# Performance work log

Hardware: AMD Instinct MI355X
Metric: run time of the kernel (lower is better)

Reference implementation:

```python
import jax, jax.numpy as jnp
import numpy as np

D_MODEL = 1024
NHEAD = 16
NUM_KV = 4
D_K = D_MODEL // NHEAD          # 64
GROUP = NHEAD // NUM_KV          # 4 query heads per kv head
ROPE_BASE = 10000.0


def _rope(x, seq_len):
    """Apply rotary embedding. x: [B, h, S, d_k], positions 0..seq_len-1."""
    half = D_K // 2
    inv_freq = 1.0 / (ROPE_BASE ** (jnp.arange(0, D_K, 2, dtype=jnp.float32) / D_K))
    t = jnp.arange(seq_len, dtype=jnp.float32)
    freqs = jnp.outer(t, inv_freq)                      # [S, d_k/2]
    emb = jnp.concatenate([freqs, freqs], axis=-1)      # [S, d_k]
    cos, sin = jnp.cos(emb), jnp.sin(emb)               # broadcast over B, h
    x1, x2 = x[..., :half], x[..., half:]
    rot = jnp.concatenate([-x2, x1], axis=-1)
    return x * cos + rot * sin


def setup_inputs() -> dict:
    key = jax.random.key(0)
    ks = jax.random.split(key, 12)
    B, S = 2, 2048
    s_in = 1.0 / np.sqrt(D_MODEL)
    inp = {
        "query": jax.random.normal(ks[0], (B, S, D_MODEL), jnp.float32),
        "key":   jax.random.normal(ks[1], (B, S, D_MODEL), jnp.float32),
        "value": jax.random.normal(ks[2], (B, S, D_MODEL), jnp.float32),
        "Wq": jax.random.normal(ks[3], (D_MODEL, D_MODEL), jnp.float32) * s_in,
        "bq": jnp.zeros((D_MODEL,), jnp.float32),
        "Wk": jax.random.normal(ks[4], (NUM_KV * D_K, D_MODEL), jnp.float32) * s_in,
        "bk": jnp.zeros((NUM_KV * D_K,), jnp.float32),
        "Wv": jax.random.normal(ks[5], (NUM_KV * D_K, D_MODEL), jnp.float32) * s_in,
        "bv": jnp.zeros((NUM_KV * D_K,), jnp.float32),
        "Wo": jax.random.normal(ks[6], (D_MODEL, D_MODEL), jnp.float32) * s_in,
        "bo": jnp.zeros((D_MODEL,), jnp.float32),
    }
    return inp


def reference(query, key, value, Wq, bq, Wk, bk, Wv, bv, Wo, bo):
    B, S, _ = query.shape
    T = key.shape[1]
    # projections (torch Linear: x @ W^T + b)
    Q = (query @ Wq.T + bq).reshape(B, S, NHEAD, D_K).transpose(0, 2, 1, 3)   # [B,H,S,dk]
    K = (key   @ Wk.T + bk).reshape(B, T, NUM_KV, D_K).transpose(0, 2, 1, 3)  # [B,KV,T,dk]
    V = (value @ Wv.T + bv).reshape(B, T, NUM_KV, D_K).transpose(0, 2, 1, 3)
    # fused RoPE (start_pos = 0)
    Q = _rope(Q, S)
    K = _rope(K, T)
    # expand kv heads (repeat_interleave on head dim)
    Kr = jnp.repeat(K, GROUP, axis=1)   # [B,H,T,dk]
    Vr = jnp.repeat(V, GROUP, axis=1)
    scale = 1.0 / np.sqrt(D_K)
    scores = jnp.einsum("bhsd,bhtd->bhst", Q, Kr) * scale   # [B,H,S,T]
    attn = jax.nn.softmax(scores, axis=-1)                    # dropout = eval/no-op
    context = jnp.einsum("bhst,bhtd->bhsd", attn, Vr)        # [B,H,S,dk]
    context = context.transpose(0, 2, 1, 3).reshape(B, S, D_MODEL)
    return context @ Wo.T + bo
```

## Files before the change

### kernel.cpp

```cpp
#include <hip/hip_runtime.h>
#include <hip/hip_bf16.h>

typedef __hip_bfloat16 bf16;
typedef __attribute__((ext_vector_type(8))) short short8;
typedef __attribute__((ext_vector_type(4))) short short4v;
typedef __attribute__((ext_vector_type(4))) float f32x4;
typedef __attribute__((ext_vector_type(4))) float float4v;

static __device__ inline short f2bf(float f){
  __hip_bfloat16 h = __float2bfloat16(f);
  return *reinterpret_cast<short*>(&h);
}

static __device__ __forceinline__ unsigned cvt_pk_bf16(float lo, float hi){
  unsigned r;
  asm("v_cvt_pk_bf16_f32 %0, %1, %2" : "=v"(r) : "v"(lo), "v"(hi));
  return r;
}

static __device__ __forceinline__ float exp2_fast(float x){
  float r;
  asm("v_exp_f32 %0, %1" : "=v"(r) : "v"(x));
  return r;
}

static __device__ __forceinline__ float max3f(float a, float b, float c){
  float r;
  asm("v_max3_f32 %0, %1, %2, %3" : "=v"(r) : "v"(a), "v"(b), "v"(c));
  return r;
}

static __device__ inline short8 load8(const float* p){
  float4v a = *reinterpret_cast<const float4v*>(p);
  float4v b = *reinterpret_cast<const float4v*>(p + 4);
  short8 r;
  unsigned* u = reinterpret_cast<unsigned*>(&r);
  u[0] = cvt_pk_bf16(a[0], a[1]);
  u[1] = cvt_pk_bf16(a[2], a[3]);
  u[2] = cvt_pk_bf16(b[0], b[1]);
  u[3] = cvt_pk_bf16(b[2], b[3]);
  return r;
}
static __device__ inline short8 load8(const bf16* p){
  return *reinterpret_cast<const short8*>(p);
}

typedef __attribute__((address_space(1))) const unsigned int gas_u32;
typedef __attribute__((address_space(3))) unsigned int las_u32;
static __device__ __forceinline__ void gload16(const void* g, void* l){
  __builtin_amdgcn_global_load_lds((gas_u32*)g, (las_u32*)l, 16, 0, 0);
}

template<int N>
static __device__ __forceinline__ void vm_barrier(){
  if constexpr (N == 8) asm volatile("s_waitcnt vmcnt(8)" ::: "memory");
  else if constexpr (N == 4) asm volatile("s_waitcnt vmcnt(4)" ::: "memory");
  else asm volatile("s_waitcnt vmcnt(0)" ::: "memory");
  __builtin_amdgcn_s_barrier();
  __builtin_amdgcn_sched_barrier(0);
}

__global__ void rope_table_kernel(float* __restrict__ tab){
  const int idx = blockIdx.x * 256 + threadIdx.x;
  const int d = idx & 31, s = idx >> 5;
  const float ang = (float)s * exp2f(-0.41524101186092030f * (float)d);
  float sn, cs;
  sincosf(ang, &sn, &cs);
  tab[idx*2] = cs; tab[idx*2+1] = sn;
}

#define CVT_Q   0
#define CVT_K   4194304
#define CVT_V   8388608
#define CVT_WQ  12582912
#define CVT_WK  13631488
#define CVT_WV  13893632
#define CVT_WO  14155776
#define CVT_TOT 15204352
__global__ void cvt_kernel(bf16* __restrict__ dst,
    const float* q, const float* k, const float* v,
    const float* wq, const float* wk, const float* wv, const float* wo){
  const size_t i8 = ((size_t)blockIdx.x * 256 + threadIdx.x) * 8;
  const float* src; size_t off;
  if      (i8 < CVT_K ){ src = q;  off = i8; }
  else if (i8 < CVT_V ){ src = k;  off = i8 - CVT_K; }
  else if (i8 < CVT_WQ){ src = v;  off = i8 - CVT_V; }
  else if (i8 < CVT_WK){ src = wq; off = i8 - CVT_WQ; }
  else if (i8 < CVT_WV){ src = wk; off = i8 - CVT_WK; }
  else if (i8 < CVT_WO){ src = wv; off = i8 - CVT_WV; }
  else                 { src = wo; off = i8 - CVT_WO; }
  *reinterpret_cast<short8*>(reinterpret_cast<short*>(dst) + i8) = load8(src + off);
}

template<int MODE>
__device__ __forceinline__ void gemm_bt_v2(
    short* lds, void* __restrict__ Cout,
    const bf16* __restrict__ A, const bf16* __restrict__ B,
    const float* __restrict__ bias, const float* __restrict__ tab,
    int ntile, int N, int K)
{
  const int NK = K >> 5;
  const int n0 = ntile * 128, m0 = blockIdx.y * 128;
  const int tid = threadIdx.x, w = tid >> 6, lane = tid & 63;
  const int wm = w >> 1, wn = w & 1, lr = lane & 15, lg = lane >> 4;
  const int r0 = w*32 + (lane >> 2), r1 = r0 + 16;
  const int c0 = ((lane & 3) ^ ((r0 >> 1) & 3)) * 8;
  const int c1 = ((lane & 3) ^ ((r1 >> 1) & 3)) * 8;
  const bf16* A0 = A + (size_t)(m0 + r0) * K + c0;
  const bf16* A1 = A + (size_t)(m0 + r1) * K + c1;
  const bf16* B0 = B + (size_t)(n0 + r0) * K + c0;
  const bf16* B1 = B + (size_t)(n0 + r1) * K + c1;
  const int ldsW = (w*32) * 32;
  int offA[4], offB[4];
  #pragma unroll
  for (int i = 0; i < 4; i++){
    const int ra = wm*64 + i*16 + lr;
    offA[i] = ra*64 + ((lg ^ ((ra >> 1) & 3)) * 16);
    const int rb = wn*64 + i*16 + lr;
    offB[i] = rb*64 + ((lg ^ ((rb >> 1) & 3)) * 16);
  }
  auto stage = [&](int t){
    short* bufA = lds + (t & 3) * 8192;
    short* bufB = bufA + 4096;
    gload16(A0 + t*32, bufA + ldsW);
    gload16(A1 + t*32, bufA + ldsW + 512);
    gload16(B0 + t*32, bufB + ldsW);
    gload16(B1 + t*32, bufB + ldsW + 512);
  };
  f32x4 acc[4][4] = {};
  stage(0); stage(1);
  for (int t = 0; t < NK; t++){
    if (t + 2 < NK){ stage(t + 2); vm_barrier<8>(); }
    else if (t + 1 < NK){ vm_barrier<4>(); }
    else { vm_barrier<0>(); }
    const char* bufA = (const char*)(lds + (t & 3) * 8192);
    const char* bufB = bufA + 8192;
    short8 af[4], bfm[4];
    #pragma unroll
    for (int mt = 0; mt < 4; mt++) af[mt]  = *(const short8*)(bufA + offA[mt]);
    #pragma unroll
    for (int nt = 0; nt < 4; nt++) bfm[nt] = *(const short8*)(bufB + offB[nt]);
    __builtin_amdgcn_s_setprio(1);
    #pragma unroll
    for (int mt = 0; mt < 4; mt++)
      #pragma unroll
      for (int nt = 0; nt < 4; nt++)
        acc[mt][nt] = __builtin_amdgcn_mfma_f32_16x16x32_bf16(af[mt], bfm[nt], acc[mt][nt], 0, 0, 0);
    __builtin_amdgcn_s_setprio(0);
  }
  if constexpr (MODE == 0){
    float* C = (float*)Cout;
    #pragma unroll
    for (int mt = 0; mt < 4; mt++){
      #pragma unroll
      for (int nt = 0; nt < 4; nt++){
        const int col = n0 + wn*64 + nt*16 + lr;
        const float bv = bias[col];
        const int rbase = m0 + wm*64 + mt*16 + lg*4;
        #pragma unroll
        for (int i = 0; i < 4; i++)
          C[(size_t)(rbase + i) * N + col] = acc[mt][nt][i] + bv;
      }
    }
  } else if constexpr (MODE == 1 || MODE == 2){
    bf16* dst = (bf16*)Cout;
    constexpr int NH = (MODE == 1) ? 16 : 4;
    constexpr float SC = (MODE == 1) ? 0.18033688011112042f : 1.0f;
    #pragma unroll
    for (int mt = 0; mt < 4; mt++){
      #pragma unroll
      for (int nt = 0; nt < 2; nt++){
        const int col = n0 + wn*64 + nt*16 + lr;
        const int d = col & 63;
        const int hh = col >> 6;
        const float b1 = bias[col], b2 = bias[col + 32];
        #pragma unroll
        for (int i = 0; i < 4; i++){
          const int m = m0 + wm*64 + mt*16 + lg*4 + i;
          const int s = m & 2047, bb = m >> 11;
          const float cs = tab[(s*32 + d)*2], sn = tab[(s*32 + d)*2 + 1];
          const float x1 = acc[mt][nt][i] + b1;
          const float x2 = acc[mt][nt+2][i] + b2;
          const size_t o = ((size_t)(bb*NH + hh) * 2048 + s) * 64 + d;
          dst[o]      = __float2bfloat16((x1*cs - x2*sn) * SC);
          dst[o + 32] = __float2bfloat16((x2*cs + x1*sn) * SC);
        }
      }
    }
  } else {
    bf16* dst = (bf16*)Cout;
    #pragma unroll
    for (int mt = 0; mt < 4; mt++){
      #pragma unroll
      for (int nt = 0; nt < 4; nt++){
        const int col = n0 + wn*64 + nt*16 + lr;
        const int kv = col >> 6, d = col & 63;
        const float bv = bias[col];
        #pragma unroll
        for (int i = 0; i < 4; i++){
          const int m = m0 + wm*64 + mt*16 + lg*4 + i;
          const int s = m & 2047, bb = m >> 11;
          dst[((size_t)(bb*4 + kv) * 64 + d) * 2048 + s] = __float2bfloat16(acc[mt][nt][i] + bv);
        }
      }
    }
  }
}

__global__ __launch_bounds__(256) void gemm_qkv_kernel(
    bf16* Qa, bf16* Ka, bf16* Va, const bf16* cvt,
    const float* bq, const float* bk, const float* bv, const float* tab){
  __shared__ short lds[4 * 8192];
  const int x = blockIdx.x;
  if (x < 8)
    gemm_bt_v2<1>(lds, Qa, cvt + CVT_Q, cvt + CVT_WQ, bq, tab, x,    1024, 1024);
  else if (x < 10)
    gemm_bt_v2<2>(lds, Ka, cvt + CVT_K, cvt + CVT_WK, bk, tab, x-8,  256, 1024);
  else
    gemm_bt_v2<3>(lds, Va, cvt + CVT_V, cvt + CVT_WV, bv, tab, x-10, 256, 1024);
}
__global__ __launch_bounds__(256) void gemm_out_kernel(
    float* C, const bf16* ctx, const bf16* cvt, const float* bo){
  __shared__ short lds[4 * 8192];
  gemm_bt_v2<0>(lds, C, ctx, cvt + CVT_WO, bo, nullptr, blockIdx.x, 1024, 1024);
}

__global__ __launch_bounds__(256) void attn_kernel(
    bf16* __restrict__ ctx, const bf16* __restrict__ Qa,
    const bf16* __restrict__ Ka, const bf16* __restrict__ Vt)
{
  __shared__ short Klds[4][64 * 64];
  __shared__ short Vlds[4][64 * 64];
  const int bh = blockIdx.y, b = bh >> 4, h = bh & 15, kvh = h >> 2;
  const int q0 = blockIdx.x * 128;
  const int tid = threadIdx.x, w = tid >> 6, lane = tid & 63;
  const int lr = lane & 15, lg = lane >> 4;
  const bf16* Qbase = Qa + (size_t)bh * 2048 * 64;
  const bf16* Kbase = Ka + (size_t)(b*4 + kvh) * 2048 * 64;
  const bf16* Vbase = Vt + (size_t)(b*4 + kvh) * 64 * 2048;

  short8 qf[2][2];
  #pragma unroll
  for (int qt = 0; qt < 2; qt++){
    qf[qt][0] = load8(Qbase + (size_t)(q0 + w*32 + qt*16 + lr) * 64 + lg*8);
    qf[qt][1] = load8(Qbase + (size_t)(q0 + w*32 + qt*16 + lr) * 64 + 32 + lg*8);
  }

  const int l8 = lane >> 3;
  const int ch = (lane & 7) ^ l8;
  const bf16* kSrc = Kbase + (size_t)(w*16 + l8) * 64 + ch*8;
  const bf16* vSrc = Vbase + (size_t)(w*16 + l8) * 2048 + ch*8;
  auto stage = [&](int bi, int t){
    short* Kd = &Klds[bi][(w*16) * 64];
    short* Vd = &Vlds[bi][(w*16) * 64];
    const bf16* ks = kSrc + (size_t)t * 64 * 64;
    const bf16* vs = vSrc + t * 64;
    gload16(ks,           Kd);
    gload16(ks + 8*64,    Kd + 8*64);
    gload16(vs,           Vd);
    gload16(vs + 8*2048,  Vd + 8*64);
  };

  float mrow[2] = {-1e30f, -1e30f}, lsum[2] = {0.f, 0.f};
  f32x4 o[2][4] = {};

  auto swzb = [](int row, int cb) -> int { return row*128 + (cb ^ ((row & 7) << 4)); };

  auto qk = [&](const char* Kc, f32x4 (&st)[4][2]){
    __builtin_amdgcn_s_setprio(1);
    #pragma unroll
    for (int mt = 0; mt < 4; mt++){
      short8 kf0 = *reinterpret_cast<const short8*>(Kc + swzb(mt*16 + lr, lg*16));
      short8 kf1 = *reinterpret_cast<const short8*>(Kc + swzb(mt*16 + lr, 64 + lg*16));
      #pragma unroll
      for (int qt = 0; qt < 2; qt++){
        st[mt][qt] = __builtin_amdgcn_mfma_f32_16x16x32_bf16(kf0, qf[qt][0], (f32x4){0.f,0.f,0.f,0.f}, 0, 0, 0);
        st[mt][qt] = __builtin_amdgcn_mfma_f32_16x16x32_bf16(kf1, qf[qt][1], st[mt][qt], 0, 0, 0);
      }
    }
    __builtin_amdgcn_s_setprio(0);
  };

  auto softmax_pv = [&](f32x4 (&st)[4][2], const char* Vc){
    short8 pf[2][2];
    #pragma unroll
    for (int qt = 0; qt < 2; qt++){
      float mx = max3f(st[0][qt][0], st[0][qt][1], st[0][qt][2]);
      mx = max3f(mx, st[0][qt][3], st[1][qt][0]);
      mx = max3f(mx, st[1][qt][1], st[1][qt][2]);
      mx = max3f(mx, st[1][qt][3], st[2][qt][0]);
      mx = max3f(mx, st[2][qt][1], st[2][qt][2]);
      mx = max3f(mx, st[2][qt][3], st[3][qt][0]);
      mx = max3f(mx, st[3][qt][1], st[3][qt][2]);
      mx = fmaxf(mx, st[3][qt][3]);
      if (__any(mx > mrow[qt] + 8.0f)){
        mx = fmaxf(mx, __shfl_xor(mx, 16));
        mx = fmaxf(mx, __shfl_xor(mx, 32));
        const float nm = fmaxf(mrow[qt], mx);
        const float alpha = exp2_fast(mrow[qt] - nm);
        mrow[qt] = nm;
        lsum[qt] *= alpha;
        float ab[4];
        #pragma unroll
        for (int i = 0; i < 4; i++) ab[i] = __shfl(alpha, lg*4 + i);
        #pragma unroll
        for (int dt = 0; dt < 4; dt++)
          #pragma unroll
          for (int i = 0; i < 4; i++)
            o[qt][dt][i] *= ab[i];
      }
      float s = 0.f;
      unsigned* pw = reinterpret_cast<unsigned*>(&pf[qt][0]);
      #pragma unroll
      for (int j = 0; j < 8; j++){
        const int mt = j >> 1, i0 = (j & 1) * 2;
        const float e0 = exp2_fast(st[mt][qt][i0]     - mrow[qt]);
        const float e1 = exp2_fast(st[mt][qt][i0 + 1] - mrow[qt]);
        pw[j] = cvt_pk_bf16(e0, e1);
        s += e0 + e1;
      }
      lsum[qt] += s;
    }
    __builtin_amdgcn_s_setprio(1);
    #pragma unroll
    for (int dt = 0; dt < 4; dt++){
      #pragma unroll
      for (int kkA = 0; kkA < 2; kkA++){
        short8 vf;
        *reinterpret_cast<short4v*>(&vf) =
            *reinterpret_cast<const short4v*>(Vc + swzb(dt*16 + lr, kkA*64 + lg*8));
        *reinterpret_cast<short4v*>(reinterpret_cast<short*>(&vf) + 4) =
            *reinterpret_cast<const short4v*>(Vc + swzb(dt*16 + lr, kkA*64 + lg*8 + 32));
        #pragma unroll
        for (int qt = 0; qt < 2; qt++)
          o[qt][dt] = __builtin_amdgcn_mfma_f32_16x16x32_bf16(pf[qt][kkA], vf, o[qt][dt], 0, 0, 0);
      }
    }
    __builtin_amdgcn_s_setprio(0);
  };

  f32x4 stA[4][2], stB[4][2];

  stage(0, 0); stage(1, 1);
  vm_barrier<4>();
  qk((const char*)&Klds[0][0], stA);

  for (int tt = 0; tt < 32; tt += 2){
    if (tt + 2 < 32){ stage((tt+2) & 3, tt+2); vm_barrier<4>(); }
    else vm_barrier<0>();
    qk((const char*)&Klds[(tt+1) & 3][0], stB);
    softmax_pv(stA, (const char*)&Vlds[tt & 3][0]);
    if (tt + 3 < 32){ stage((tt+3) & 3, tt+3); vm_barrier<4>(); }
    else vm_barrier<0>();
    if (tt + 2 < 32) qk((const char*)&Klds[(tt+2) & 3][0], stA);
    softmax_pv(stB, (const char*)&Vlds[(tt+1) & 3][0]);
  }

  #pragma unroll
  for (int qt = 0; qt < 2; qt++){
    float s = lsum[qt];
    s += __shfl_xor(s, 16);
    s += __shfl_xor(s, 32);
    float lb[4];
    #pragma unroll
    for (int i = 0; i < 4; i++) lb[i] = 1.0f / __shfl(s, lg*4 + i);
    #pragma unroll
    for (int dt = 0; dt < 4; dt++){
      #pragma unroll
      for (int i = 0; i < 4; i++){
        const int q = q0 + w*32 + qt*16 + lg*4 + i;
        ctx[(size_t)(b*2048 + q) * 1024 + h*64 + dt*16 + lr] =
            __float2bfloat16(o[qt][dt][i] * lb[i]);
      }
    }
  }
}

extern "C" void kernel_launch(void* const* d_in, const int* in_sizes, int n_in,
                              void* d_out, int out_size, void* d_ws, size_t ws_size,
                              hipStream_t stream)
{
  const float* query = (const float*)d_in[0];
  const float* key   = (const float*)d_in[1];
  const float* value = (const float*)d_in[2];
  const float* Wq = (const float*)d_in[3];
  const float* bq = (const float*)d_in[4];
  const float* Wk = (const float*)d_in[5];
  const float* bk = (const float*)d_in[6];
  const float* Wv = (const float*)d_in[7];
  const float* bv = (const float*)d_in[8];
  const float* Wo = (const float*)d_in[9];
  const float* bo = (const float*)d_in[10];
  float* out = (float*)d_out;

  char* ws = (char*)d_ws;
  size_t off = 0;
  float* tab = (float*)(ws + off); off += (size_t)2048 * 32 * 2 * 4;
  bf16*  Qa  = (bf16*)(ws + off);  off += (size_t)32 * 2048 * 64 * 2;
  bf16*  Ka  = (bf16*)(ws + off);  off += (size_t)8 * 2048 * 64 * 2;
  bf16*  Va  = (bf16*)(ws + off);  off += (size_t)8 * 64 * 2048 * 2;
  bf16*  ctx = (bf16*)(ws + off);  off += (size_t)2 * 2048 * 1024 * 2;
  bf16*  cvt = (bf16*)(ws + off);  off += (size_t)CVT_TOT * 2;

  rope_table_kernel<<<256, 256, 0, stream>>>(tab);
  cvt_kernel<<<CVT_TOT / 8 / 256, 256, 0, stream>>>(cvt, query, key, value, Wq, Wk, Wv, Wo);
  gemm_qkv_kernel<<<dim3(12, 32), 256, 0, stream>>>(Qa, Ka, Va, cvt, bq, bk, bv, tab);
  attn_kernel<<<dim3(16, 32), 256, 0, stream>>>(ctx, Qa, Ka, Va);
  gemm_out_kernel<<<dim3(8, 32), 256, 0, stream>>>(out, ctx, cvt, bo);
}
```

Measured before the change: 120.4 us.

## Fold rope table into cvt kernel, compute softmax row sums via MFMA, precompute LDS offsets

Removes the separate rope-table launch by computing the sin/cos table inside the first 256 blocks of the conversion kernel. In attention, the row-sum of softmax probabilities now comes from an MFMA against a vector of bf16 ones instead of scalar adds and cross-lane shuffles, so it is computed from the same bf16-rounded probabilities used for PV. Swizzled LDS offsets are precomputed once, the max reduction is rebalanced into a shallower tree, and launch bounds now request 2 blocks per CU for the three main kernels. The extra MFMAs and register-pressure caps could offset some of the savings.

```diff
diff --git a/kernel.cpp b/kernel.cpp
--- a/kernel.cpp
+++ b/kernel.cpp
@@ -55,18 +55,10 @@
 static __device__ __forceinline__ void vm_barrier(){
   if constexpr (N == 8) asm volatile("s_waitcnt vmcnt(8)" ::: "memory");
   else if constexpr (N == 4) asm volatile("s_waitcnt vmcnt(4)" ::: "memory");
+  else if constexpr (N == 2) asm volatile("s_waitcnt vmcnt(2)" ::: "memory");
   else asm volatile("s_waitcnt vmcnt(0)" ::: "memory");
   __builtin_amdgcn_s_barrier();
   __builtin_amdgcn_sched_barrier(0);
-}
-
-__global__ void rope_table_kernel(float* __restrict__ tab){
-  const int idx = blockIdx.x * 256 + threadIdx.x;
-  const int d = idx & 31, s = idx >> 5;
-  const float ang = (float)s * exp2f(-0.41524101186092030f * (float)d);
-  float sn, cs;
-  sincosf(ang, &sn, &cs);
-  tab[idx*2] = cs; tab[idx*2+1] = sn;
 }
 
 #define CVT_Q   0
@@ -77,9 +69,17 @@
 #define CVT_WV  13893632
 #define CVT_WO  14155776
 #define CVT_TOT 15204352
-__global__ void cvt_kernel(bf16* __restrict__ dst,
+__global__ void cvt_kernel(bf16* __restrict__ dst, float* __restrict__ tab,
     const float* q, const float* k, const float* v,
     const float* wq, const float* wk, const float* wv, const float* wo){
+  if (blockIdx.x < 256){
+    const int idx = blockIdx.x * 256 + threadIdx.x;
+    const int d = idx & 31, s = idx >> 5;
+    const float ang = (float)s * exp2f(-0.41524101186092030f * (float)d);
+    float sn, cs;
+    sincosf(ang, &sn, &cs);
+    tab[idx*2] = cs; tab[idx*2+1] = sn;
+  }
   const size_t i8 = ((size_t)blockIdx.x * 256 + threadIdx.x) * 8;
   const float* src; size_t off;
   if      (i8 < CVT_K ){ src = q;  off = i8; }
@@ -207,7 +207,7 @@
   }
 }
 
-__global__ __launch_bounds__(256) void gemm_qkv_kernel(
+__global__ __launch_bounds__(256, 2) void gemm_qkv_kernel(
     bf16* Qa, bf16* Ka, bf16* Va, const bf16* cvt,
     const float* bq, const float* bk, const float* bv, const float* tab){
   __shared__ short lds[4 * 8192];
@@ -219,13 +219,13 @@
   else
     gemm_bt_v2<3>(lds, Va, cvt + CVT_V, cvt + CVT_WV, bv, tab, x-10, 256, 1024);
 }
-__global__ __launch_bounds__(256) void gemm_out_kernel(
+__global__ __launch_bounds__(256, 2) void gemm_out_kernel(
     float* C, const bf16* ctx, const bf16* cvt, const float* bo){
   __shared__ short lds[4 * 8192];
   gemm_bt_v2<0>(lds, C, ctx, cvt + CVT_WO, bo, nullptr, blockIdx.x, 1024, 1024);
 }
 
-__global__ __launch_bounds__(256) void attn_kernel(
+__global__ __launch_bounds__(256, 2) void attn_kernel(
     bf16* __restrict__ ctx, const bf16* __restrict__ Qa,
     const bf16* __restrict__ Ka, const bf16* __restrict__ Vt)
 {
@@ -245,6 +245,16 @@
     qf[qt][0] = load8(Qbase + (size_t)(q0 + w*32 + qt*16 + lr) * 64 + lg*8);
     qf[qt][1] = load8(Qbase + (size_t)(q0 + w*32 + qt*16 + lr) * 64 + 32 + lg*8);
   }
+
+  const int xsw = (lr & 7) << 4;
+  const int koff0 = lr*128 + ((lg*16) ^ xsw);
+  const int koff1 = lr*128 + ((64 + lg*16) ^ xsw);
+  int voff[2][2];
+  #pragma unroll
+  for (int kkA = 0; kkA < 2; kkA++)
+    #pragma unroll
+    for (int hh = 0; hh < 2; hh++)
+      voff[kkA][hh] = lr*128 + ((kkA*64 + lg*8 + hh*32) ^ xsw);
 
   const int l8 = lane >> 3;
   const int ch = (lane & 7) ^ l8;
@@ -261,17 +271,19 @@
     gload16(vs + 8*2048,  Vd + 8*64);
   };
 
-  float mrow[2] = {-1e30f, -1e30f}, lsum[2] = {0.f, 0.f};
+  float mrow[2] = {-1e30f, -1e30f};
   f32x4 o[2][4] = {};
-
-  auto swzb = [](int row, int cb) -> int { return row*128 + (cb ^ ((row & 7) << 4)); };
+  f32x4 acc_l[2] = {};
+  short8 ones;
+  #pragma unroll
+  for (int j = 0; j < 4; j++) reinterpret_cast<unsigned*>(&ones)[j] = 0x3F803F80u;
 
   auto qk = [&](const char* Kc, f32x4 (&st)[4][2]){
     __builtin_amdgcn_s_setprio(1);
     #pragma unroll
     for (int mt = 0; mt < 4; mt++){
-      short8 kf0 = *reinterpret_cast<const short8*>(Kc + swzb(mt*16 + lr, lg*16));
-      short8 kf1 = *reinterpret_cast<const short8*>(Kc + swzb(mt*16 + lr, 64 + lg*16));
+      short8 kf0 = *reinterpret_cast<const short8*>(Kc + mt*2048 + koff0);
+      short8 kf1 = *reinterpret_cast<const short8*>(Kc + mt*2048 + koff1);
       #pragma unroll
       for (int qt = 0; qt < 2; qt++){
         st[mt][qt] = __builtin_amdgcn_mfma_f32_16x16x32_bf16(kf0, qf[qt][0], (f32x4){0.f,0.f,0.f,0.f}, 0, 0, 0);
@@ -285,21 +297,18 @@
     short8 pf[2][2];
     #pragma unroll
     for (int qt = 0; qt < 2; qt++){
-      float mx = max3f(st[0][qt][0], st[0][qt][1], st[0][qt][2]);
-      mx = max3f(mx, st[0][qt][3], st[1][qt][0]);
-      mx = max3f(mx, st[1][qt][1], st[1][qt][2]);
-      mx = max3f(mx, st[1][qt][3], st[2][qt][0]);
-      mx = max3f(mx, st[2][qt][1], st[2][qt][2]);
-      mx = max3f(mx, st[2][qt][3], st[3][qt][0]);
-      mx = max3f(mx, st[3][qt][1], st[3][qt][2]);
-      mx = fmaxf(mx, st[3][qt][3]);
+      const float m0 = max3f(st[0][qt][0], st[0][qt][1], st[0][qt][2]);
+      const float m1 = max3f(st[0][qt][3], st[1][qt][0], st[1][qt][1]);
+      const float m2 = max3f(st[1][qt][2], st[1][qt][3], st[2][qt][0]);
+      const float m3 = max3f(st[2][qt][1], st[2][qt][2], st[2][qt][3]);
+      const float m4 = max3f(st[3][qt][0], st[3][qt][1], st[3][qt][2]);
+      float mx = fmaxf(max3f(m0, m1, m2), max3f(m3, m4, st[3][qt][3]));
       if (__any(mx > mrow[qt] + 8.0f)){
         mx = fmaxf(mx, __shfl_xor(mx, 16));
         mx = fmaxf(mx, __shfl_xor(mx, 32));
         const float nm = fmaxf(mrow[qt], mx);
         const float alpha = exp2_fast(mrow[qt] - nm);
         mrow[qt] = nm;
-        lsum[qt] *= alpha;
         float ab[4];
         #pragma unroll
         for (int i = 0; i < 4; i++) ab[i] = __shfl(alpha, lg*4 + i);
@@ -308,8 +317,9 @@
           #pragma unroll
           for (int i = 0; i < 4; i++)
             o[qt][dt][i] *= ab[i];
-      }
-      float s = 0.f;
+        #pragma unroll
+        for (int i = 0; i < 4; i++) acc_l[qt][i] *= ab[i];
+      }
       unsigned* pw = reinterpret_cast<unsigned*>(&pf[qt][0]);
       #pragma unroll
       for (int j = 0; j < 8; j++){
@@ -317,20 +327,23 @@
         const float e0 = exp2_fast(st[mt][qt][i0]     - mrow[qt]);
         const float e1 = exp2_fast(st[mt][qt][i0 + 1] - mrow[qt]);
         pw[j] = cvt_pk_bf16(e0, e1);
-        s += e0 + e1;
-      }
-      lsum[qt] += s;
+      }
     }
     __builtin_amdgcn_s_setprio(1);
+    #pragma unroll
+    for (int qt = 0; qt < 2; qt++){
+      acc_l[qt] = __builtin_amdgcn_mfma_f32_16x16x32_bf16(pf[qt][0], ones, acc_l[qt], 0, 0, 0);
+      acc_l[qt] = __builtin_amdgcn_mfma_f32_16x16x32_bf16(pf[qt][1], ones, acc_l[qt], 0, 0, 0);
+    }
     #pragma unroll
     for (int dt = 0; dt < 4; dt++){
       #pragma unroll
       for (int kkA = 0; kkA < 2; kkA++){
         short8 vf;
         *reinterpret_cast<short4v*>(&vf) =
-            *reinterpret_cast<const short4v*>(Vc + swzb(dt*16 + lr, kkA*64 + lg*8));
+            *reinterpret_cast<const short4v*>(Vc + dt*2048 + voff[kkA][0]);
         *reinterpret_cast<short4v*>(reinterpret_cast<short*>(&vf) + 4) =
-            *reinterpret_cast<const short4v*>(Vc + swzb(dt*16 + lr, kkA*64 + lg*8 + 32));
+            *reinterpret_cast<const short4v*>(Vc + dt*2048 + voff[kkA][1]);
         #pragma unroll
         for (int qt = 0; qt < 2; qt++)
           o[qt][dt] = __builtin_amdgcn_mfma_f32_16x16x32_bf16(pf[qt][kkA], vf, o[qt][dt], 0, 0, 0);
@@ -358,12 +371,9 @@
 
   #pragma unroll
   for (int qt = 0; qt < 2; qt++){
-    float s = lsum[qt];
-    s += __shfl_xor(s, 16);
-    s += __shfl_xor(s, 32);
     float lb[4];
     #pragma unroll
-    for (int i = 0; i < 4; i++) lb[i] = 1.0f / __shfl(s, lg*4 + i);
+    for (int i = 0; i < 4; i++) lb[i] = 1.0f / acc_l[qt][i];
     #pragma unroll
     for (int dt = 0; dt < 4; dt++){
       #pragma unroll
@@ -402,8 +412,7 @@
   bf16*  ctx = (bf16*)(ws + off);  off += (size_t)2 * 2048 * 1024 * 2;
   bf16*  cvt = (bf16*)(ws + off);  off += (size_t)CVT_TOT * 2;
 
-  rope_table_kernel<<<256, 256, 0, stream>>>(tab);
-  cvt_kernel<<<CVT_TOT / 8 / 256, 256, 0, stream>>>(cvt, query, key, value, Wq, Wk, Wv, Wo);
+  cvt_kernel<<<CVT_TOT / 8 / 256, 256, 0, stream>>>(cvt, tab, query, key, value, Wq, Wk, Wv, Wo);
   gemm_qkv_kernel<<<dim3(12, 32), 256, 0, stream>>>(Qa, Ka, Va, cvt, bq, bk, bv, tab);
   attn_kernel<<<dim3(16, 32), 256, 0, stream>>>(ctx, Qa, Ka, Va);
   gemm_out_kernel<<<dim3(8, 32), 256, 0, stream>>>(out, ctx, cvt, bo);
```

Measured after the change: 106.5 us. -11.5%, faster.
